# Performance work log

Measured on AMD Instinct MI355X. Metric: run time of the kernel, lower is better.

Reference implementation:

```python
import jax, jax.numpy as jnp
import numpy as np

T, B, N, C, H = 4, 4, 1024, 512, 8
D = C // H
EPS = 1e-5
TAU = 2.0
SCALE = 0.125


def _bn(x, g, b, m, v):
    # eval-mode BatchNorm1d over channel dim C (last axis here)
    return (x - m) * jax.lax.rsqrt(v + EPS) * g + b


def _lif(x, v_th=1.0):
    # multi-step LIF over leading T axis: v += (x - v)/tau; spike = H(v - vth);
    # hard reset to 0 (detach_reset); sigmoid surrogate (alpha=4) straight-through
    def step(v, xt):
        v = v + (xt - v) / TAU
        sg = jax.nn.sigmoid(4.0 * (v - v_th))
        hard = (v >= v_th).astype(x.dtype)
        spike = sg + jax.lax.stop_gradient(hard - sg)
        v = v * (1.0 - jax.lax.stop_gradient(spike))
        return v, spike
    _, s = jax.lax.scan(step, jnp.zeros_like(x[0]), x)
    return s


def _heads(y):
    # [T,B,N,C] -> [T,B,H,N,D]
    return y.reshape(T, B, N, H, D).transpose(0, 1, 3, 2, 4)


def _forward(x, s_x, q_w, q_b, q_g, q_bt, q_m, q_v,
             k_w, k_b, k_g, k_bt, k_m, k_v,
             v_w, v_b, v_g, v_bt, v_m, v_v,
             p_w, p_b, p_g, p_bt, p_m, p_v):
    # s_x is flattened but never used in the original forward
    q = _heads(_lif(_bn(x @ q_w.T + q_b, q_g, q_bt, q_m, q_v)))
    k = _heads(_lif(_bn(x @ k_w.T + k_b, k_g, k_bt, k_m, k_v)))
    v = _heads(_bn(x @ v_w.T + v_b, v_g, v_bt, v_m, v_v))  # no v_lif in original forward
    attn = jnp.einsum('tbhnd,tbhmd->tbhnm', q, k) * SCALE
    o = jnp.einsum('tbhnm,tbhmd->tbhnd', attn, v)
    o = o.transpose(0, 1, 3, 2, 4).reshape(T, B, N, C)
    return _bn(o @ p_w.T + p_b, p_g, p_bt, p_m, p_v)


def setup_inputs() -> dict:
    key = jax.random.key(0)
    ks = jax.random.split(key, 10)
    def w(k):
        return jax.random.normal(k, (C, C), jnp.float32) * 0.02
    ones = jnp.ones((C,), jnp.float32)
    zeros = jnp.zeros((C,), jnp.float32)
    return {
        'x': jax.random.normal(ks[0], (T, B, N, C), jnp.float32),
        's_x': jax.random.normal(ks[1], (T, B, N, C), jnp.float32),
        'q_w': w(ks[2]), 'q_b': zeros,
        'q_g': jax.random.uniform(ks[6], (C,), jnp.float32, 0.5, 1.5), 'q_bt': zeros, 'q_m': zeros, 'q_v': ones,
        'k_w': w(ks[3]), 'k_b': zeros,
        'k_g': jax.random.uniform(ks[7], (C,), jnp.float32, 0.5, 1.5), 'k_bt': zeros, 'k_m': zeros, 'k_v': ones,
        'v_w': w(ks[4]), 'v_b': zeros,
        'v_g': jax.random.uniform(ks[8], (C,), jnp.float32, 0.5, 1.5), 'v_bt': zeros, 'v_m': zeros, 'v_v': ones,
        'p_w': w(ks[5]), 'p_b': zeros,
        'p_g': jax.random.uniform(ks[9], (C,), jnp.float32, 0.5, 1.5), 'p_bt': zeros, 'p_m': zeros, 'p_v': ones,
    }


def reference(x, s_x, q_w, q_b, q_g, q_bt, q_m, q_v,
              k_w, k_b, k_g, k_bt, k_m, k_v,
              v_w, v_b, v_g, v_bt, v_m, v_v,
              p_w, p_b, p_g, p_bt, p_m, p_v):
    return _forward(x, s_x, q_w, q_b, q_g, q_bt, q_m, q_v,
                    k_w, k_b, k_g, k_bt, k_m, k_v,
                    v_w, v_b, v_g, v_bt, v_m, v_v,
                    p_w, p_b, p_g, p_bt, p_m, p_v)
```

## Files before the change

### kernel.cpp

```cpp
#include <hip/hip_runtime.h>


#define T_ 4
#define B_ 4
#define N_ 1024
#define C_ 512
#define H_ 8
#define M_ (T_*B_*N_)

typedef __bf16 bf16x8 __attribute__((ext_vector_type(8)));
typedef float  floatx4 __attribute__((ext_vector_type(4)));

__device__ __forceinline__ float bf2f(unsigned short u) {
  union { unsigned int i; float f; } v; v.i = ((unsigned int)u) << 16; return v.f;
}
__device__ __forceinline__ unsigned short f2bf(float f) {
  unsigned int x = __float_as_uint(f);
  return (unsigned short)((x + 0x7fffu + ((x >> 16) & 1u)) >> 16);
}

#define GLOAD16(gaddr, ldsbase) \
  __builtin_amdgcn_global_load_lds((__attribute__((address_space(1))) void*)(gaddr), \
                                   (__attribute__((address_space(3))) void*)(ldsbase), 16, 0, 0)

struct BnParams { const float* p[20]; };
struct PrepArgs {
  const float *x, *qw, *kw, *vw, *pw;
  unsigned short *X2, *Wqk3, *Wvb, *Wpb;
  float *scl, *sft;
  BnParams bp;
};

__global__ __launch_bounds__(256) void prep_all(PrepArgs P) {
  const int bid = blockIdx.x;
  if (bid < 8192) {
    const int idx = (bid * 256 + threadIdx.x) * 4;
    const float4 v = *(const float4*)(P.x + idx);
    const int m = idx >> 9, k = idx & 511;
    const int t = m >> 12, b = (m >> 10) & 3, n = m & 1023;
    const int mp = (((b << 10) | n) << 2) | t;
    const size_t base = (size_t)mp * 1024 + k;
    float vv[4] = {v.x, v.y, v.z, v.w};
    unsigned short h[4], l[4];
#pragma unroll
    for (int j = 0; j < 4; ++j) { h[j] = f2bf(vv[j]); l[j] = f2bf(vv[j] - bf2f(h[j])); }
    *(ushort4*)(P.X2 + base) = ushort4{h[0], h[1], h[2], h[3]};
    *(ushort4*)(P.X2 + base + 512) = ushort4{l[0], l[1], l[2], l[3]};
  } else if (bid < 9216) {
    const int z = (bid - 8192) >> 8;
    const int idx = ((((bid - 8192) & 255) * 256) + threadIdx.x) * 4;
    const float* src = (z == 0) ? P.qw : (z == 1) ? P.kw : (z == 2) ? P.vw : P.pw;
    const float4 v = *(const float4*)(src + idx);
    if (z >= 2) {
      unsigned short* dst = (z == 2) ? P.Wvb : P.Wpb;
      *(ushort4*)(dst + idx) = ushort4{f2bf(v.x), f2bf(v.y), f2bf(v.z), f2bf(v.w)};
      return;
    }
    const int row = idx >> 9, k = idx & 511;
    unsigned short* dst = P.Wqk3 + (size_t)(z * 512) * 1536;
    const size_t base = (size_t)row * 1536 + k;
    float vv[4] = {v.x, v.y, v.z, v.w};
    unsigned short h[4], l[4];
#pragma unroll
    for (int j = 0; j < 4; ++j) { h[j] = f2bf(vv[j]); l[j] = f2bf(vv[j] - bf2f(h[j])); }
    ushort4 hi{h[0], h[1], h[2], h[3]};
    *(ushort4*)(dst + base) = hi;
    *(ushort4*)(dst + base + 512) = hi;
    *(ushort4*)(dst + base + 1024) = ushort4{l[0], l[1], l[2], l[3]};
  } else {
    const int o = (bid - 9216) * 256 + threadIdx.x;
    const int grp = o >> 9, ci = o & 511;
    const float s = P.bp.p[grp * 5 + 1][ci] * rsqrtf(P.bp.p[grp * 5 + 4][ci] + 1e-5f);
    P.scl[o] = s;
    P.sft[o] = (P.bp.p[grp * 5 + 0][ci] - P.bp.p[grp * 5 + 3][ci]) * s + P.bp.p[grp * 5 + 2][ci];
  }
}

struct Job2 {
  const unsigned short* A; int lda;
  const unsigned short* w; int ldb;
  int K, ldc, epi;
  const float* scl; const float* sft;
  float* out32; unsigned short* out16; unsigned short* out16b;
};

__device__ __forceinline__ void qk_body(const Job2& job, int bx,
                                        unsigned short (*AB)[256 * 64]) {
  const int xcd = bx & 7, slot = bx >> 3;
  const int panel = xcd + 8 * (slot >> 2);
  const int m0 = panel * 256;
  const int n0 = (slot & 3) * 256;

  const int tid = threadIdx.x;
  const int wv = tid >> 6, lane = tid & 63;
  const int wm = wv >> 1, wn = wv & 1;
  const int NT = job.K >> 5;

  const int rloc = lane >> 3;
  const int ulog = (lane & 7) ^ rloc;
  const bool isA = ulog < 4;
  const unsigned short* bq[4];
#pragma unroll
  for (int q = 0; q < 4; ++q) {
    const int row = wv * 32 + q * 8 + rloc;
    bq[q] = isA ? job.A + (size_t)(m0 + row) * job.lda + ulog * 8
                : job.w + (size_t)(n0 + row) * job.ldb + (ulog - 4) * 8;
  }

#define ISSUE(T_, BUF_) do {                                                 \
    const int t_ = (T_);                                                     \
    const int off_ = isA ? ((t_ < 32 ? t_ : t_ - 32) << 5) : (t_ << 5);      \
    _Pragma("unroll")                                                        \
    for (int q = 0; q < 4; ++q)                                              \
      GLOAD16(bq[q] + off_, &AB[BUF_][(wv * 32 + q * 8) * 64]);              \
  } while (0)

  const int r15 = lane & 15;
  const int apos = (lane >> 4) ^ (lane & 7);
  const int bpos = (4 | (lane >> 4)) ^ (lane & 7);
  const int aoff = (wm * 64 + r15) * 64 + apos * 8;
  const int boff = (wn * 128 + r15) * 64 + bpos * 8;

  bf16x8 A0[4], A1[4], L0[4], L1[4], Hh[4];

#define RD_A_L01(BUF_, AX, LX) do {                                          \
    const unsigned short* lb_ = &AB[BUF_][0];                                \
    _Pragma("unroll")                                                        \
    for (int i_ = 0; i_ < 4; ++i_) AX[i_] = *(const bf16x8*)(lb_ + aoff + i_ * 1024); \
    LX[0] = *(const bf16x8*)(lb_ + boff);                                    \
    LX[1] = *(const bf16x8*)(lb_ + boff + 1024);                             \
  } while (0)

#define RD_L23_HI(BUF_, LX) do {                                             \
    const unsigned short* lb_ = &AB[BUF_][0];                                \
    LX[2] = *(const bf16x8*)(lb_ + boff + 2 * 1024);                         \
    LX[3] = *(const bf16x8*)(lb_ + boff + 3 * 1024);                         \
    _Pragma("unroll")                                                        \
    for (int j_ = 0; j_ < 4; ++j_) Hh[j_] = *(const bf16x8*)(lb_ + boff + (4 + j_) * 1024); \
  } while (0)

#define MF_LO(AX, LX) do {                                                   \
    __builtin_amdgcn_s_setprio(1);                                           \
    _Pragma("unroll")                                                        \
    for (int j_ = 0; j_ < 4; ++j_)                                           \
    _Pragma("unroll")                                                        \
      for (int i_ = 0; i_ < 4; ++i_)                                         \
        acc[i_][j_] = __builtin_amdgcn_mfma_f32_16x16x32_bf16(AX[i_], LX[j_], acc[i_][j_], 0, 0, 0); \
    __builtin_amdgcn_s_setprio(0);                                           \
  } while (0)

#define MF_HI(AX) do {                                                       \
    __builtin_amdgcn_s_setprio(1);                                           \
    _Pragma("unroll")                                                        \
    for (int i_ = 0; i_ < 4; ++i_)                                           \
    _Pragma("unroll")                                                        \
      for (int j_ = 0; j_ < 4; ++j_)                                         \
        acc[i_][4 + j_] = __builtin_amdgcn_mfma_f32_16x16x32_bf16(AX[i_], Hh[j_], acc[i_][4 + j_], 0, 0, 0); \
    __builtin_amdgcn_s_setprio(0);                                           \
  } while (0)

#define MIDBAR(N_) do {                                                      \
    asm volatile("s_waitcnt vmcnt(" #N_ ")" ::: "memory");                   \
    __builtin_amdgcn_s_barrier();                                            \
    __builtin_amdgcn_sched_barrier(0);                                       \
  } while (0)

#define SLOT_I(KT_, BC_, BN_, AX, LX, AY, LY) do {                           \
    RD_L23_HI(BC_, LX); MF_LO(AX, LX);                                       \
    MIDBAR(8);                                                               \
    ISSUE((KT_) + 4, BC_);                                                   \
    RD_A_L01(BN_, AY, LY); MF_HI(AX);                                        \
  } while (0)

  floatx4 acc[4][8];
#pragma unroll
  for (int i = 0; i < 4; ++i)
#pragma unroll
    for (int j = 0; j < 8; ++j) acc[i][j] = floatx4{0.f, 0.f, 0.f, 0.f};

  ISSUE(0, 0); ISSUE(1, 1); ISSUE(2, 2); ISSUE(3, 3);
  asm volatile("s_waitcnt vmcnt(12)" ::: "memory");
  __builtin_amdgcn_s_barrier();
  __builtin_amdgcn_sched_barrier(0);
  RD_A_L01(0, A0, L0);

  const int NG = (NT - 4) >> 2;
  for (int g = 0; g < NG; ++g) {
    const int g4 = g << 2;
    SLOT_I(g4 + 0, 0, 1, A0, L0, A1, L1);
    SLOT_I(g4 + 1, 1, 2, A1, L1, A0, L0);
    SLOT_I(g4 + 2, 2, 3, A0, L0, A1, L1);
    SLOT_I(g4 + 3, 3, 0, A1, L1, A0, L0);
  }
  RD_L23_HI(0, L0); MF_LO(A0, L0); MIDBAR(8); RD_A_L01(1, A1, L1); MF_HI(A0);
  RD_L23_HI(1, L1); MF_LO(A1, L1); MIDBAR(4); RD_A_L01(2, A0, L0); MF_HI(A1);
  RD_L23_HI(2, L0); MF_LO(A0, L0); MIDBAR(0); RD_A_L01(3, A1, L1); MF_HI(A0);
  RD_L23_HI(3, L1); MF_LO(A1, L1); MF_HI(A1);

  float scl[8], sft[8];
#pragma unroll
  for (int j = 0; j < 8; ++j) {
    const int c = n0 + wn * 128 + j * 16 + r15;
    scl[j] = job.scl[c];
    sft[j] = job.sft[c];
  }
  const int rbase = m0 + wm * 64 + (lane >> 4) * 4;

  if (n0 < 512) {
    const int cb = n0 + wn * 128 + r15;
#pragma unroll
    for (int i = 0; i < 4; ++i) {
      unsigned short spk[4][8];
#pragma unroll
      for (int j = 0; j < 8; ++j) {
        float vme = 0.f;
#pragma unroll
        for (int r = 0; r < 4; ++r) {
          const float y = acc[i][j][r] * scl[j] + sft[j];
          vme += (y - vme) * 0.5f;
          const bool sp = vme >= 1.0f;
          spk[r][j] = sp ? (unsigned short)0x3F80 : (unsigned short)0;
          if (sp) vme = 0.f;
        }
      }
#pragma unroll
      for (int r = 0; r < 4; ++r) {
        unsigned short* prow = job.out16 + (size_t)(rbase + 16 * i + r) * 512 + cb;
#pragma unroll
        for (int j = 0; j < 8; ++j) prow[j * 16] = spk[r][j];
      }
    }
  } else {
    __syncthreads();
    unsigned short* lds = &AB[0][0];
    const int gq = lane >> 4;
#pragma unroll
    for (int i = 0; i < 4; ++i) {
      const int n_loc = wm * 16 + 4 * i + gq;
#pragma unroll
      for (int j = 0; j < 8; ++j) {
        const int c_loc = wn * 128 + j * 16 + r15;
        const int colbase = c_loc * 64 + (n_loc ^ ((c_loc & 7) << 3));
        float vme = 0.f;
#pragma unroll
        for (int r = 0; r < 4; ++r) {
          const float y = acc[i][j][r] * scl[j] + sft[j];
          vme += (y - vme) * 0.5f;
          const bool sp = vme >= 1.0f;
          lds[r * 16384 + colbase] = sp ? (unsigned short)0x3F80 : (unsigned short)0;
          if (sp) vme = 0.f;
        }
      }
    }
    __syncthreads();
    const int b = panel >> 4, n0g = (panel & 15) * 64, cb = n0 - 512;
#pragma unroll
    for (int it = 0; it < 16; ++it) {
      const int rho = wv * 128 + it * 8 + (lane >> 3);
      const int t = rho >> 8, c = rho & 255;
      const int nb = lane & 7;
      const uint4 d = *(const uint4*)&lds[t * 16384 + c * 64 + ((nb ^ (c & 7)) << 3)];
      *(uint4*)(job.out16b + (size_t)((t * 4 + b) * 512 + cb + c) * 1024 + n0g + nb * 8) = d;
    }
  }
}

__device__ __forceinline__ void v_body(const Job2& job, int bx,
                                       unsigned short (*ABS)[384 * 32]) {
  const int xcd = bx & 7, slot = bx >> 3;
  const int panel = xcd + 8 * (slot >> 1);
  const int m0 = panel * 128;
  const int n0 = (slot & 1) * 256;

  const int tid = threadIdx.x;
  const int wv = tid >> 6, lane = tid & 63;
  const int wm = wv >> 2, wn = wv & 3;

  const unsigned short* src[3];
#pragma unroll
  for (int g = 0; g < 3; ++g) {
    const int row = wv * 48 + g * 16 + (lane >> 2);
    const int ulog = (lane & 3) ^ (row & 3);
    src[g] = (row < 128) ? job.A + (size_t)(m0 + row) * job.lda + ulog * 8
                         : job.w + (size_t)(n0 + row - 128) * job.ldb + ulog * 8;
  }

#define ISSUE1(T_, BUF_) do {                                                \
    const int k0_ = (T_) << 5;                                               \
    _Pragma("unroll")                                                        \
    for (int g_ = 0; g_ < 3; ++g_)                                           \
      GLOAD16(src[g_] + k0_, &ABS[BUF_][(wv * 48 + g_ * 16) * 32]);          \
  } while (0)

  const int r15 = lane & 15;
  const int uoff = ((lane >> 4) ^ (r15 & 3)) << 3;
  const int arow0 = (wm * 64 + r15) * 32 + uoff;
  const int brow0 = (128 + wn * 64 + r15) * 32 + uoff;

  bf16x8 AX[4], BX[4], AY[4], BY[4];
#define RD1(BUF_, A_, B_) do {                                               \
    const unsigned short* lb_ = &ABS[BUF_][0];                               \
    _Pragma("unroll")                                                        \
    for (int i_ = 0; i_ < 4; ++i_) A_[i_] = *(const bf16x8*)(lb_ + arow0 + i_ * 512); \
    _Pragma("unroll")                                                        \
    for (int j_ = 0; j_ < 4; ++j_) B_[j_] = *(const bf16x8*)(lb_ + brow0 + j_ * 512); \
  } while (0)

#define MF1(A_, B_) do {                                                     \
    __builtin_amdgcn_s_setprio(1);                                           \
    _Pragma("unroll")                                                        \
    for (int i_ = 0; i_ < 4; ++i_)                                           \
    _Pragma("unroll")                                                        \
      for (int j_ = 0; j_ < 4; ++j_)                                         \
        acc[i_][j_] = __builtin_amdgcn_mfma_f32_16x16x32_bf16(A_[i_], B_[j_], acc[i_][j_], 0, 0, 0); \
    __builtin_amdgcn_s_setprio(0);                                           \
  } while (0)

#define MB1(N_) do {                                                         \
    asm volatile("s_waitcnt vmcnt(" #N_ ")" ::: "memory");                   \
    __builtin_amdgcn_s_barrier();                                            \
    __builtin_amdgcn_sched_barrier(0);                                       \
  } while (0)

  floatx4 acc[4][4];
#pragma unroll
  for (int i = 0; i < 4; ++i)
#pragma unroll
    for (int j = 0; j < 4; ++j) acc[i][j] = floatx4{0.f, 0.f, 0.f, 0.f};

  ISSUE1(0, 0); ISSUE1(1, 1); ISSUE1(2, 2); ISSUE1(3, 3);
  asm volatile("s_waitcnt vmcnt(9)" ::: "memory");
  __builtin_amdgcn_s_barrier();
  __builtin_amdgcn_sched_barrier(0);
  RD1(0, AX, BX);

#pragma unroll 1
  for (int kt = 0; kt < 12; kt += 2) {
    MB1(6); ISSUE1(kt + 4, kt & 3);       RD1((kt + 1) & 3, AY, BY); MF1(AX, BX);
    MB1(6); ISSUE1(kt + 5, (kt + 1) & 3); RD1((kt + 2) & 3, AX, BX); MF1(AY, BY);
  }
  MB1(6); RD1(1, AY, BY); MF1(AX, BX);
  MB1(3); RD1(2, AX, BX); MF1(AY, BY);
  MB1(0); RD1(3, AY, BY); MF1(AX, BX);
  MF1(AY, BY);

  float scl[4], sft[4];
#pragma unroll
  for (int j = 0; j < 4; ++j) {
    const int c = n0 + wn * 64 + j * 16 + r15;
    scl[j] = job.scl[c];
    sft[j] = job.sft[c];
  }
  const int rbase = m0 + wm * 64 + (lane >> 4) * 4;

  if (job.epi == 4) {
    __syncthreads();
    unsigned short* lds = &ABS[0][0];
    const int gq = lane >> 4;
#pragma unroll
    for (int i = 0; i < 4; ++i) {
      const int n_loc = wm * 16 + 4 * i + gq;
#pragma unroll
      for (int j = 0; j < 4; ++j) {
        const int c_loc = wn * 64 + j * 16 + r15;
        const int colbase = c_loc * 32 + (n_loc ^ (((c_loc >> 2) & 3) << 3));
#pragma unroll
        for (int r = 0; r < 4; ++r)
          lds[r * 8192 + colbase] = f2bf(acc[i][j][r] * scl[j] + sft[j]);
      }
    }
    __syncthreads();
    const int b = panel >> 5, n0g = (panel & 31) * 32;
#pragma unroll
    for (int it = 0; it < 8; ++it) {
      const int rho = wv * 128 + it * 16 + (lane >> 2);
      const int t = rho >> 8, c = rho & 255;
      const int nb = lane & 3;
      const uint4 d = *(const uint4*)&lds[t * 8192 + c * 32 + ((nb ^ ((c >> 2) & 3)) << 3)];
      *(uint4*)(job.out16b + (size_t)((t * 4 + b) * 512 + n0 + c) * 1024 + n0g + nb * 8) = d;
    }
  } else {
#pragma unroll
    for (int i = 0; i < 4; ++i)
#pragma unroll
      for (int r = 0; r < 4; ++r) {
        const int mp = rbase + 16 * i + r;
        const int t = mp & 3, bn = mp >> 2;
        const int mstd = (((t << 2) | (bn >> 10)) << 10) | (bn & 1023);
        float* prow = job.out32 + (size_t)mstd * 512 + n0 + wn * 64 + r15;
#pragma unroll
        for (int j = 0; j < 4; ++j) prow[j * 16] = acc[i][j][r] * scl[j] + sft[j];
      }
  }
}

__global__ __launch_bounds__(512, 2) void gemm_fused(Job2 jqk, Job2 jv) {
  __shared__ unsigned short AB[4][256 * 64];
  if (blockIdx.x < 256) qk_body(jqk, blockIdx.x, AB);
  else                  v_body(jv, blockIdx.x - 256, (unsigned short (*)[384 * 32])AB);
}

__global__ __launch_bounds__(512, 2) void gemm128(Job2 job) {
  __shared__ unsigned short ABS[4][384 * 32];
  v_body(job, blockIdx.x, ABS);
}

__global__ __launch_bounds__(256) void kv_gemm(const unsigned short* __restrict__ ktr,
                                               const unsigned short* __restrict__ vtr,
                                               unsigned short* __restrict__ kvt) {
  const int head = blockIdx.x;
  const int tb = head >> 3;
  const int h = head & 7;
  const int wv = threadIdx.x >> 6, lane = threadIdx.x & 63;
  const int m0 = wv * 256;
  const size_t cbase = (size_t)tb * C_ + h * 64;
  const int rsel = lane & 15, koff = (lane >> 4) * 8;

  floatx4 acc[4][4];
#pragma unroll
  for (int i = 0; i < 4; ++i)
#pragma unroll
    for (int j = 0; j < 4; ++j) acc[i][j] = floatx4{0.f, 0.f, 0.f, 0.f};

#pragma unroll
  for (int s = 0; s < 8; ++s) {
    const int m = m0 + s * 32 + koff;
    bf16x8 a[4], b[4];
#pragma unroll
    for (int dt = 0; dt < 4; ++dt)
      a[dt] = *(const bf16x8*)(ktr + (cbase + dt * 16 + rsel) * N_ + m);
#pragma unroll
    for (int et = 0; et < 4; ++et)
      b[et] = *(const bf16x8*)(vtr + (cbase + et * 16 + rsel) * N_ + m);
#pragma unroll
    for (int dt = 0; dt < 4; ++dt)
#pragma unroll
      for (int et = 0; et < 4; ++et)
        acc[dt][et] = __builtin_amdgcn_mfma_f32_16x16x32_bf16(a[dt], b[et], acc[dt][et], 0, 0, 0);
  }

  __shared__ float red[4096];
  const int dbase = (lane >> 4) * 4;
  const int e0 = lane & 15;
#pragma unroll 1
  for (int w = 0; w < 4; ++w) {
    if (wv == w) {
#pragma unroll
      for (int dt = 0; dt < 4; ++dt)
#pragma unroll
        for (int et = 0; et < 4; ++et)
#pragma unroll
          for (int r = 0; r < 4; ++r) {
            const int o = (dt * 16 + dbase + r) * 64 + et * 16 + e0;
            red[o] = (w == 0) ? acc[dt][et][r] : red[o] + acc[dt][et][r];
          }
    }
    __syncthreads();
  }
  const int d = threadIdx.x & 63;
  const int eg = threadIdx.x >> 6;
#pragma unroll
  for (int j = 0; j < 16; ++j) {
    const int e = eg * 16 + j;
    kvt[(size_t)head * 4096 + e * 64 + d] = f2bf(0.125f * red[d * 64 + e]);
  }
}

__global__ __launch_bounds__(256) void av_gemm(const unsigned short* __restrict__ qs,
                                               const unsigned short* __restrict__ kvt,
                                               unsigned short* __restrict__ obuf) {
  const int bx = blockIdx.x;
  const int tb = bx >> 4;
  const int sub = bx & 15;
  const int nt = sub >> 1;
  const int h0 = (sub & 1) * 4;
  const int t = tb >> 2, b = tb & 3;
  const int wv = threadIdx.x >> 6, lane = threadIdx.x & 63;
  const int n0 = nt * 128 + wv * 32;
  const int rsel = lane & 15, koff = (lane >> 4) * 8;

#pragma unroll 1
  for (int h = h0; h < h0 + 4; ++h) {
    floatx4 acc[2][4];
#pragma unroll
    for (int i = 0; i < 2; ++i)
#pragma unroll
      for (int j = 0; j < 4; ++j) acc[i][j] = floatx4{0.f, 0.f, 0.f, 0.f};
    const unsigned short* kvh = kvt + ((size_t)tb * 8 + h) * 4096;
#pragma unroll
    for (int s = 0; s < 2; ++s) {
      bf16x8 a[2], bv[4];
#pragma unroll
      for (int i = 0; i < 2; ++i) {
        const int n = n0 + i * 16 + rsel;
        a[i] = *(const bf16x8*)(qs + (size_t)((((b << 10) | n) << 2) | t) * 512 + h * 64 + s * 32 + koff);
      }
#pragma unroll
      for (int et = 0; et < 4; ++et)
        bv[et] = *(const bf16x8*)(kvh + (et * 16 + rsel) * 64 + s * 32 + koff);
#pragma unroll
      for (int i = 0; i < 2; ++i)
#pragma unroll
        for (int et = 0; et < 4; ++et)
          acc[i][et] = __builtin_amdgcn_mfma_f32_16x16x32_bf16(a[i], bv[et], acc[i][et], 0, 0, 0);
    }
#pragma unroll
    for (int i = 0; i < 2; ++i)
#pragma unroll
      for (int et = 0; et < 4; ++et)
#pragma unroll
        for (int r = 0; r < 4; ++r) {
          const int n = n0 + i * 16 + (lane >> 4) * 4 + r;
          obuf[(size_t)((((b << 10) | n) << 2) | t) * 512 + h * 64 + et * 16 + rsel] = f2bf(acc[i][et][r]);
        }
  }
}

extern "C" void kernel_launch(void* const* d_in, const int* in_sizes, int n_in,
                              void* d_out, int out_size, void* d_ws, size_t ws_size,
                              hipStream_t stream) {
  char* ws = (char*)d_ws;
  unsigned short* X2   = (unsigned short*)(ws + 0);
  unsigned short* Wqk3 = (unsigned short*)(ws + 33554432ull);
  unsigned short* Wvb  = (unsigned short*)(ws + 36700160ull);
  unsigned short* Wpb  = (unsigned short*)(ws + 37224448ull);
  float*          scl  = (float*)(ws + 37748736ull);
  float*          sft  = (float*)(ws + 37756928ull);
  unsigned short* qsb  = (unsigned short*)(ws + 41943040ull);
  unsigned short* ktr  = (unsigned short*)(ws + 58720256ull);
  unsigned short* vtr  = (unsigned short*)(ws + 75497472ull);
  unsigned short* kvt  = (unsigned short*)(ws + 92274688ull);
  unsigned short* ob   = (unsigned short*)(ws + 93323264ull);

  PrepArgs pa;
  pa.x  = (const float*)d_in[0];
  pa.qw = (const float*)d_in[2];
  pa.kw = (const float*)d_in[8];
  pa.vw = (const float*)d_in[14];
  pa.pw = (const float*)d_in[20];
  pa.X2 = X2; pa.Wqk3 = Wqk3; pa.Wvb = Wvb; pa.Wpb = Wpb;
  pa.scl = scl; pa.sft = sft;
  pa.bp.p[0]=(const float*)d_in[3];  pa.bp.p[1]=(const float*)d_in[4];  pa.bp.p[2]=(const float*)d_in[5];  pa.bp.p[3]=(const float*)d_in[6];  pa.bp.p[4]=(const float*)d_in[7];
  pa.bp.p[5]=(const float*)d_in[9];  pa.bp.p[6]=(const float*)d_in[10]; pa.bp.p[7]=(const float*)d_in[11]; pa.bp.p[8]=(const float*)d_in[12]; pa.bp.p[9]=(const float*)d_in[13];
  pa.bp.p[10]=(const float*)d_in[15];pa.bp.p[11]=(const float*)d_in[16];pa.bp.p[12]=(const float*)d_in[17];pa.bp.p[13]=(const float*)d_in[18];pa.bp.p[14]=(const float*)d_in[19];
  pa.bp.p[15]=(const float*)d_in[21];pa.bp.p[16]=(const float*)d_in[22];pa.bp.p[17]=(const float*)d_in[23];pa.bp.p[18]=(const float*)d_in[24];pa.bp.p[19]=(const float*)d_in[25];
  prep_all<<<dim3(9224), 256, 0, stream>>>(pa);

  Job2 jqk{X2, 1024, Wqk3, 1536, 1536, 512, 2, scl, sft, nullptr, qsb, ktr};
  Job2 jv {X2, 1024, Wvb,  512,  512,  512, 4, scl + 1024, sft + 1024, nullptr, nullptr, vtr};
  gemm_fused<<<dim3(512), 512, 0, stream>>>(jqk, jv);

  kv_gemm<<<dim3(128), 256, 0, stream>>>(ktr, vtr, kvt);
  av_gemm<<<dim3(256), 256, 0, stream>>>(qsb, kvt, ob);

  Job2 jp{ob, 512, Wpb, 512, 512, 512, 3, scl + 1536, sft + 1536, (float*)d_out, nullptr, nullptr};
  gemm128<<<dim3(256), 512, 0, stream>>>(jp);
}
```

Baseline: 122.1 us.

## Load GEMM B operand directly from global into registers instead of LDS

The weight (B) fragments are now read with per-lane global loads straight into registers, one k-tile ahead, instead of being staged through LDS alongside A. This removes the LDS read traffic and bank pressure for B and frees the LDS reads to serve only A. In exchange it doubles B register usage (two 8-fragment buffers), exposes global latency that the vmcnt waits now have to cover, and leaves the ISSUE macro still staging B into LDS unless it was changed elsewhere.

```diff
diff --git a/kernel.cpp b/kernel.cpp
--- a/kernel.cpp
+++ b/kernel.cpp
@@ -116,46 +116,46 @@
   } while (0)
 
   const int r15 = lane & 15;
+  const int koff = (lane >> 4) * 8;
   const int apos = (lane >> 4) ^ (lane & 7);
-  const int bpos = (4 | (lane >> 4)) ^ (lane & 7);
   const int aoff = (wm * 64 + r15) * 64 + apos * 8;
-  const int boff = (wn * 128 + r15) * 64 + bpos * 8;
-
-  bf16x8 A0[4], A1[4], L0[4], L1[4], Hh[4];
-
-#define RD_A_L01(BUF_, AX, LX) do {                                          \
+
+  const unsigned short* wb[8];
+#pragma unroll
+  for (int j = 0; j < 8; ++j)
+    wb[j] = job.w + (size_t)(n0 + wn * 128 + j * 16 + r15) * job.ldb + koff;
+
+  bf16x8 A0[4], A1[4], B0[8], B1[8];
+
+#define RD_A(BUF_, AX) do {                                                  \
     const unsigned short* lb_ = &AB[BUF_][0];                                \
     _Pragma("unroll")                                                        \
     for (int i_ = 0; i_ < 4; ++i_) AX[i_] = *(const bf16x8*)(lb_ + aoff + i_ * 1024); \
-    LX[0] = *(const bf16x8*)(lb_ + boff);                                    \
-    LX[1] = *(const bf16x8*)(lb_ + boff + 1024);                             \
-  } while (0)
-
-#define RD_L23_HI(BUF_, LX) do {                                             \
-    const unsigned short* lb_ = &AB[BUF_][0];                                \
-    LX[2] = *(const bf16x8*)(lb_ + boff + 2 * 1024);                         \
-    LX[3] = *(const bf16x8*)(lb_ + boff + 3 * 1024);                         \
-    _Pragma("unroll")                                                        \
-    for (int j_ = 0; j_ < 4; ++j_) Hh[j_] = *(const bf16x8*)(lb_ + boff + (4 + j_) * 1024); \
-  } while (0)
-
-#define MF_LO(AX, LX) do {                                                   \
+  } while (0)
+
+#define LOADB(T_, BV) do {                                                   \
+    const int kB_ = (T_) << 5;                                               \
+    _Pragma("unroll")                                                        \
+    for (int j_ = 0; j_ < 8; ++j_) BV[j_] = *(const bf16x8*)(wb[j_] + kB_);  \
+  } while (0)
+
+#define MF_LO(AX, BV) do {                                                   \
     __builtin_amdgcn_s_setprio(1);                                           \
     _Pragma("unroll")                                                        \
     for (int j_ = 0; j_ < 4; ++j_)                                           \
     _Pragma("unroll")                                                        \
       for (int i_ = 0; i_ < 4; ++i_)                                         \
-        acc[i_][j_] = __builtin_amdgcn_mfma_f32_16x16x32_bf16(AX[i_], LX[j_], acc[i_][j_], 0, 0, 0); \
+        acc[i_][j_] = __builtin_amdgcn_mfma_f32_16x16x32_bf16(AX[i_], BV[j_], acc[i_][j_], 0, 0, 0); \
     __builtin_amdgcn_s_setprio(0);                                           \
   } while (0)
 
-#define MF_HI(AX) do {                                                       \
+#define MF_HI(AX, BV) do {                                                   \
     __builtin_amdgcn_s_setprio(1);                                           \
     _Pragma("unroll")                                                        \
     for (int i_ = 0; i_ < 4; ++i_)                                           \
     _Pragma("unroll")                                                        \
       for (int j_ = 0; j_ < 4; ++j_)                                         \
-        acc[i_][4 + j_] = __builtin_amdgcn_mfma_f32_16x16x32_bf16(AX[i_], Hh[j_], acc[i_][4 + j_], 0, 0, 0); \
+        acc[i_][4 + j_] = __builtin_amdgcn_mfma_f32_16x16x32_bf16(AX[i_], BV[4 + j_], acc[i_][4 + j_], 0, 0, 0); \
     __builtin_amdgcn_s_setprio(0);                                           \
   } while (0)
 
@@ -165,11 +165,11 @@
     __builtin_amdgcn_sched_barrier(0);                                       \
   } while (0)
 
-#define SLOT_I(KT_, BC_, BN_, AX, LX, AY, LY) do {                           \
-    RD_L23_HI(BC_, LX); MF_LO(AX, LX);                                       \
-    MIDBAR(8);                                                               \
+#define SLOT_I(KT_, BC_, BN_, AX, BX, AY, BY) do {                           \
+    LOADB((KT_) + 1, BY); MF_LO(AX, BX);                                     \
+    MIDBAR(32);                                                              \
     ISSUE((KT_) + 4, BC_);                                                   \
-    RD_A_L01(BN_, AY, LY); MF_HI(AX);                                        \
+    RD_A(BN_, AY); MF_HI(AX, BX);                                            \
   } while (0)
 
   floatx4 acc[4][8];
@@ -178,24 +178,25 @@
 #pragma unroll
     for (int j = 0; j < 8; ++j) acc[i][j] = floatx4{0.f, 0.f, 0.f, 0.f};
 
+  LOADB(0, B0);
   ISSUE(0, 0); ISSUE(1, 1); ISSUE(2, 2); ISSUE(3, 3);
   asm volatile("s_waitcnt vmcnt(12)" ::: "memory");
   __builtin_amdgcn_s_barrier();
   __builtin_amdgcn_sched_barrier(0);
-  RD_A_L01(0, A0, L0);
+  RD_A(0, A0);
 
   const int NG = (NT - 4) >> 2;
   for (int g = 0; g < NG; ++g) {
     const int g4 = g << 2;
-    SLOT_I(g4 + 0, 0, 1, A0, L0, A1, L1);
-    SLOT_I(g4 + 1, 1, 2, A1, L1, A0, L0);
-    SLOT_I(g4 + 2, 2, 3, A0, L0, A1, L1);
-    SLOT_I(g4 + 3, 3, 0, A1, L1, A0, L0);
-  }
-  RD_L23_HI(0, L0); MF_LO(A0, L0); MIDBAR(8); RD_A_L01(1, A1, L1); MF_HI(A0);
-  RD_L23_HI(1, L1); MF_LO(A1, L1); MIDBAR(4); RD_A_L01(2, A0, L0); MF_HI(A1);
-  RD_L23_HI(2, L0); MF_LO(A0, L0); MIDBAR(0); RD_A_L01(3, A1, L1); MF_HI(A0);
-  RD_L23_HI(3, L1); MF_LO(A1, L1); MF_HI(A1);
+    SLOT_I(g4 + 0, 0, 1, A0, B0, A1, B1);
+    SLOT_I(g4 + 1, 1, 2, A1, B1, A0, B0);
+    SLOT_I(g4 + 2, 2, 3, A0, B0, A1, B1);
+    SLOT_I(g4 + 3, 3, 0, A1, B1, A0, B0);
+  }
+  LOADB(NT - 3, B1); MF_LO(A0, B0); MIDBAR(32); RD_A(1, A1); MF_HI(A0, B0);
+  LOADB(NT - 2, B0); MF_LO(A1, B1); MIDBAR(28); RD_A(2, A0); MF_HI(A1, B1);
+  LOADB(NT - 1, B1); MF_LO(A0, B0); MIDBAR(24); RD_A(3, A1); MF_HI(A0, B0);
+  MF_LO(A1, B1); MF_HI(A1, B1);
 
   float scl[8], sft[8];
 #pragma unroll
```

Result: slower. 198.0 us (+62.1%).

## Split GEMM k-slot into four interleaved MFMA/LDS-read phases with explicit waitcnts

Applied to the files above, without the earlier changes.

Restructures each k-step of the GEMM main loop into four phases. Each phase issues a small batch of LDS fragment reads, waits with an explicit lgkmcnt, runs eight MFMAs and hits a workgroup barrier. The goal is a finer interleave of LDS reads with MFMA work and staggered waves, so fewer MFMAs sit waiting on LDS. In exchange it adds three more barriers per k-step and hand-tuned waitcnt counts that could serialize the loop if they are wrong.

```diff
diff --git a/kernel.cpp b/kernel.cpp
--- a/kernel.cpp
+++ b/kernel.cpp
@@ -123,53 +123,67 @@
 
   bf16x8 A0[4], A1[4], L0[4], L1[4], Hh[4];
 
-#define RD_A_L01(BUF_, AX, LX) do {                                          \
-    const unsigned short* lb_ = &AB[BUF_][0];                                \
-    _Pragma("unroll")                                                        \
-    for (int i_ = 0; i_ < 4; ++i_) AX[i_] = *(const bf16x8*)(lb_ + aoff + i_ * 1024); \
-    LX[0] = *(const bf16x8*)(lb_ + boff);                                    \
-    LX[1] = *(const bf16x8*)(lb_ + boff + 1024);                             \
-  } while (0)
-
-#define RD_L23_HI(BUF_, LX) do {                                             \
-    const unsigned short* lb_ = &AB[BUF_][0];                                \
-    LX[2] = *(const bf16x8*)(lb_ + boff + 2 * 1024);                         \
-    LX[3] = *(const bf16x8*)(lb_ + boff + 3 * 1024);                         \
-    _Pragma("unroll")                                                        \
-    for (int j_ = 0; j_ < 4; ++j_) Hh[j_] = *(const bf16x8*)(lb_ + boff + (4 + j_) * 1024); \
-  } while (0)
-
-#define MF_LO(AX, LX) do {                                                   \
+#define LGKM(N_) do {                                                        \
+    asm volatile("s_waitcnt lgkmcnt(" #N_ ")" ::: "memory");                 \
+    __builtin_amdgcn_sched_barrier(0);                                       \
+  } while (0)
+
+#define VMC(N_) do {                                                         \
+    asm volatile("s_waitcnt vmcnt(" #N_ ")" ::: "memory");                   \
+    __builtin_amdgcn_sched_barrier(0);                                       \
+  } while (0)
+
+#define BAR __builtin_amdgcn_s_barrier()
+
+#define MFPAIR(AX, J0_, F0_, F1_) do {                                       \
     __builtin_amdgcn_s_setprio(1);                                           \
     _Pragma("unroll")                                                        \
+    for (int i_ = 0; i_ < 4; ++i_)                                           \
+      acc[i_][J0_] = __builtin_amdgcn_mfma_f32_16x16x32_bf16(AX[i_], F0_, acc[i_][J0_], 0, 0, 0); \
+    _Pragma("unroll")                                                        \
+    for (int i_ = 0; i_ < 4; ++i_)                                           \
+      acc[i_][(J0_) + 1] = __builtin_amdgcn_mfma_f32_16x16x32_bf16(AX[i_], F1_, acc[i_][(J0_) + 1], 0, 0, 0); \
+    __builtin_amdgcn_s_setprio(0);                                           \
+  } while (0)
+
+#define SLOT4(KT_, BC_, BN_, AX, LX, AY, LY) do {                            \
+    const unsigned short* lbc_ = &AB[BC_][0];                                \
+    const unsigned short* lbn_ = &AB[BN_][0];                                \
+    LX[2] = *(const bf16x8*)(lbc_ + boff + 2048);                            \
+    LX[3] = *(const bf16x8*)(lbc_ + boff + 3072);                            \
+    LGKM(2); MFPAIR(AX, 0, LX[0], LX[1]); BAR;                               \
+    _Pragma("unroll")                                                        \
     for (int j_ = 0; j_ < 4; ++j_)                                           \
-    _Pragma("unroll")                                                        \
-      for (int i_ = 0; i_ < 4; ++i_)                                         \
-        acc[i_][j_] = __builtin_amdgcn_mfma_f32_16x16x32_bf16(AX[i_], LX[j_], acc[i_][j_], 0, 0, 0); \
-    __builtin_amdgcn_s_setprio(0);                                           \
-  } while (0)
-
-#define MF_HI(AX) do {                                                       \
-    __builtin_amdgcn_s_setprio(1);                                           \
+      Hh[j_] = *(const bf16x8*)(lbc_ + boff + (4 + j_) * 1024);              \
+    LGKM(4); MFPAIR(AX, 2, LX[2], LX[3]); BAR;                               \
+    VMC(8); ISSUE((KT_) + 4, BC_);                                           \
     _Pragma("unroll")                                                        \
     for (int i_ = 0; i_ < 4; ++i_)                                           \
-    _Pragma("unroll")                                                        \
-      for (int j_ = 0; j_ < 4; ++j_)                                         \
-        acc[i_][4 + j_] = __builtin_amdgcn_mfma_f32_16x16x32_bf16(AX[i_], Hh[j_], acc[i_][4 + j_], 0, 0, 0); \
-    __builtin_amdgcn_s_setprio(0);                                           \
-  } while (0)
-
-#define MIDBAR(N_) do {                                                      \
-    asm volatile("s_waitcnt vmcnt(" #N_ ")" ::: "memory");                   \
-    __builtin_amdgcn_s_barrier();                                            \
-    __builtin_amdgcn_sched_barrier(0);                                       \
-  } while (0)
-
-#define SLOT_I(KT_, BC_, BN_, AX, LX, AY, LY) do {                           \
-    RD_L23_HI(BC_, LX); MF_LO(AX, LX);                                       \
-    MIDBAR(8);                                                               \
-    ISSUE((KT_) + 4, BC_);                                                   \
-    RD_A_L01(BN_, AY, LY); MF_HI(AX);                                        \
+      AY[i_] = *(const bf16x8*)(lbn_ + aoff + i_ * 1024);                    \
+    LGKM(4); MFPAIR(AX, 4, Hh[0], Hh[1]); BAR;                               \
+    LY[0] = *(const bf16x8*)(lbn_ + boff);                                   \
+    LY[1] = *(const bf16x8*)(lbn_ + boff + 1024);                            \
+    MFPAIR(AX, 6, Hh[2], Hh[3]); BAR;                                        \
+  } while (0)
+
+#define SLOT4T(BC_, BN_, AX, LX, AY, LY, VM_) do {                           \
+    const unsigned short* lbc_ = &AB[BC_][0];                                \
+    const unsigned short* lbn_ = &AB[BN_][0];                                \
+    LX[2] = *(const bf16x8*)(lbc_ + boff + 2048);                            \
+    LX[3] = *(const bf16x8*)(lbc_ + boff + 3072);                            \
+    LGKM(2); MFPAIR(AX, 0, LX[0], LX[1]); BAR;                               \
+    _Pragma("unroll")                                                        \
+    for (int j_ = 0; j_ < 4; ++j_)                                           \
+      Hh[j_] = *(const bf16x8*)(lbc_ + boff + (4 + j_) * 1024);              \
+    LGKM(4); MFPAIR(AX, 2, LX[2], LX[3]); BAR;                               \
+    VMC(VM_);                                                                \
+    _Pragma("unroll")                                                        \
+    for (int i_ = 0; i_ < 4; ++i_)                                           \
+      AY[i_] = *(const bf16x8*)(lbn_ + aoff + i_ * 1024);                    \
+    LGKM(4); MFPAIR(AX, 4, Hh[0], Hh[1]); BAR;                               \
+    LY[0] = *(const bf16x8*)(lbn_ + boff);                                   \
+    LY[1] = *(const bf16x8*)(lbn_ + boff + 1024);                            \
+    MFPAIR(AX, 6, Hh[2], Hh[3]); BAR;                                        \
   } while (0)
 
   floatx4 acc[4][8];
@@ -179,23 +193,39 @@
     for (int j = 0; j < 8; ++j) acc[i][j] = floatx4{0.f, 0.f, 0.f, 0.f};
 
   ISSUE(0, 0); ISSUE(1, 1); ISSUE(2, 2); ISSUE(3, 3);
-  asm volatile("s_waitcnt vmcnt(12)" ::: "memory");
-  __builtin_amdgcn_s_barrier();
-  __builtin_amdgcn_sched_barrier(0);
-  RD_A_L01(0, A0, L0);
+  VMC(12);
+  BAR;
+  {
+    const unsigned short* lb0 = &AB[0][0];
+#pragma unroll
+    for (int i = 0; i < 4; ++i) A0[i] = *(const bf16x8*)(lb0 + aoff + i * 1024);
+    L0[0] = *(const bf16x8*)(lb0 + boff);
+    L0[1] = *(const bf16x8*)(lb0 + boff + 1024);
+  }
 
   const int NG = (NT - 4) >> 2;
   for (int g = 0; g < NG; ++g) {
     const int g4 = g << 2;
-    SLOT_I(g4 + 0, 0, 1, A0, L0, A1, L1);
-    SLOT_I(g4 + 1, 1, 2, A1, L1, A0, L0);
-    SLOT_I(g4 + 2, 2, 3, A0, L0, A1, L1);
-    SLOT_I(g4 + 3, 3, 0, A1, L1, A0, L0);
-  }
-  RD_L23_HI(0, L0); MF_LO(A0, L0); MIDBAR(8); RD_A_L01(1, A1, L1); MF_HI(A0);
-  RD_L23_HI(1, L1); MF_LO(A1, L1); MIDBAR(4); RD_A_L01(2, A0, L0); MF_HI(A1);
-  RD_L23_HI(2, L0); MF_LO(A0, L0); MIDBAR(0); RD_A_L01(3, A1, L1); MF_HI(A0);
-  RD_L23_HI(3, L1); MF_LO(A1, L1); MF_HI(A1);
+    SLOT4(g4 + 0, 0, 1, A0, L0, A1, L1);
+    SLOT4(g4 + 1, 1, 2, A1, L1, A0, L0);
+    SLOT4(g4 + 2, 2, 3, A0, L0, A1, L1);
+    SLOT4(g4 + 3, 3, 0, A1, L1, A0, L0);
+  }
+  SLOT4T(0, 1, A0, L0, A1, L1, 8);
+  SLOT4T(1, 2, A1, L1, A0, L0, 4);
+  SLOT4T(2, 3, A0, L0, A1, L1, 0);
+  {
+    const unsigned short* lbc_ = &AB[3][0];
+    L1[2] = *(const bf16x8*)(lbc_ + boff + 2048);
+    L1[3] = *(const bf16x8*)(lbc_ + boff + 3072);
+    LGKM(2); MFPAIR(A1, 0, L1[0], L1[1]);
+#pragma unroll
+    for (int j_ = 0; j_ < 4; ++j_)
+      Hh[j_] = *(const bf16x8*)(lbc_ + boff + (4 + j_) * 1024);
+    LGKM(4); MFPAIR(A1, 2, L1[2], L1[3]);
+    LGKM(0); MFPAIR(A1, 4, Hh[0], Hh[1]);
+    MFPAIR(A1, 6, Hh[2], Hh[3]);
+  }
 
   float scl[8], sft[8];
 #pragma unroll
```

New measurement: 123.9 us. About the same (+1.4%).
